# Kernel tuning notes

Measured on AMD Instinct MI355X. Metric: run time of the kernel, lower is better.

## Reference

```python
import jax, jax.numpy as jnp
import numpy as np
from jax import lax

LRELU = 0.1
SQRT_HALF = 0.7071067811865476
DIM = 128
NUM_PRE = 5          # dilated convs in UpsampleNet
NUM_BLOCKS = 3       # WaveNet blocks
LAYERS_PER_BLOCK = 10
NUM_WN = NUM_BLOCKS * LAYERS_PER_BLOCK  # 30


def conv1d(x, w, b, dilation=1):
    # x: [N,C,L], w: [O,I,K], 'same' padding for odd K
    k = w.shape[-1]
    pad = dilation * (k // 2)
    y = lax.conv_general_dilated(
        x, w, window_strides=(1,), padding=[(pad, pad)],
        rhs_dilation=(dilation,), dimension_numbers=('NCW', 'OIW', 'NCW'))
    return y + b[None, :, None]


def conv_transpose1d(x, w, b, stride=4):
    # kernel 4, stride 4, no padding -> L_out = 4*L
    y = lax.conv_transpose(
        x, w, strides=(stride,), padding='VALID',
        dimension_numbers=('NCW', 'OIW', 'NCW'))
    return y + b[None, :, None]


def setup_inputs() -> dict:
    key = jax.random.key(0)
    ks = iter(jax.random.split(key, 32))
    s = 0.02
    d = {}
    d['mel'] = jax.random.normal(next(ks), (4, 80, 64), jnp.float32)
    d['in_w'] = s * jax.random.normal(next(ks), (DIM, 80, 1), jnp.float32)
    d['in_b'] = jnp.zeros((DIM,), jnp.float32)
    d['pre_ws'] = s * jax.random.normal(next(ks), (NUM_PRE, DIM, DIM, 3), jnp.float32)
    d['pre_bs'] = jnp.zeros((NUM_PRE, DIM), jnp.float32)
    d['up1_w'] = s * jax.random.normal(next(ks), (DIM, DIM, 4), jnp.float32)
    d['up1_b'] = jnp.zeros((DIM,), jnp.float32)
    d['up2_w'] = s * jax.random.normal(next(ks), (DIM, DIM, 4), jnp.float32)
    d['up2_b'] = jnp.zeros((DIM,), jnp.float32)
    d['wn_ws'] = s * jax.random.normal(next(ks), (NUM_WN, 2 * DIM, DIM, 3), jnp.float32)
    d['wn_bs'] = jnp.zeros((NUM_WN, 2 * DIM), jnp.float32)
    d['sk_ws'] = s * jax.random.normal(next(ks), (NUM_WN, DIM, DIM, 1), jnp.float32)
    d['sk_bs'] = jnp.zeros((NUM_WN, DIM), jnp.float32)
    d['out1_w'] = s * jax.random.normal(next(ks), (DIM, DIM, 1), jnp.float32)
    d['out1_b'] = jnp.zeros((DIM,), jnp.float32)
    d['out2_w'] = s * jax.random.normal(next(ks), (DIM, DIM, 1), jnp.float32)
    d['out2_b'] = jnp.zeros((DIM,), jnp.float32)
    d['out3_w'] = s * jax.random.normal(next(ks), (1, DIM, 1), jnp.float32)
    d['out3_b'] = jnp.zeros((1,), jnp.float32)
    return d


def reference(mel, in_w, in_b, pre_ws, pre_bs, up1_w, up1_b, up2_w, up2_b,
              wn_ws, wn_bs, sk_ws, sk_bs,
              out1_w, out1_b, out2_w, out2_b, out3_w, out3_b):
    # ---- UpsampleNet ----
    x = conv1d(mel, in_w, in_b)                       # [N,128,T]
    for i in range(NUM_PRE):
        residual = x
        x = conv1d(x, pre_ws[i], pre_bs[i], dilation=2 ** i)
        x = jax.nn.leaky_relu(x, LRELU)
        x = (x + residual) * SQRT_HALF
    x = jax.nn.leaky_relu(conv_transpose1d(x, up1_w, up1_b), LRELU)
    x = jax.nn.leaky_relu(conv_transpose1d(x, up2_w, up2_b), LRELU)
    N, D, L = x.shape
    x = jnp.broadcast_to(x[:, :, :, None], (N, D, L, 16)).reshape(N, D, L * 16)

    # ---- WaveNet blocks (3 blocks x 10 layers) ----
    skips = jnp.zeros_like(x)
    for li in range(NUM_WN):
        dilation = 2 ** (li % LAYERS_PER_BLOCK)
        residual = x
        g = conv1d(x, wn_ws[li], wn_bs[li], dilation=dilation)  # [N,256,L]
        g_tanh, g_sig = jnp.split(g, 2, axis=1)
        gated = jnp.tanh(g_tanh) * jax.nn.sigmoid(g_sig)
        s = conv1d(gated, sk_ws[li], sk_bs[li])
        skips = skips + s
        x = s + residual

    # ---- Output stack ----
    y = jax.nn.relu(skips)
    y = jax.nn.relu(conv1d(y, out1_w, out1_b))
    y = jax.nn.relu(conv1d(y, out2_w, out2_b))
    y = conv1d(y, out3_w, out3_b)
    return jnp.tanh(y)  # [N,1,L*256]
```

## Files before the change

### kernel.cpp

```cpp
#include <hip/hip_runtime.h>
#include <math.h>

#define LRELU 0.1f
#define SQRT_HALF 0.7071067811865476f

constexpr int T_LEN = 16384;

typedef __attribute__((ext_vector_type(8))) short short8;
typedef __attribute__((ext_vector_type(4))) float f32x4;

union U4S8 { uint4 v; short8 s8; unsigned short us[8]; };

__device__ inline void bsplit(float v, unsigned short& hi, unsigned short& lo) {
    unsigned u = __float_as_uint(v);
    unsigned rh = (u + 0x7FFFu + ((u >> 16) & 1u)) >> 16;
    float fh = __uint_as_float(rh << 16);
    float r = v - fh;
    unsigned u2 = __float_as_uint(r);
    unsigned rl = (u2 + 0x7FFFu + ((u2 >> 16) & 1u)) >> 16;
    hi = (unsigned short)rh; lo = (unsigned short)rl;
}
__device__ inline float b2f(unsigned short s) { return __uint_as_float(((unsigned)s) << 16); }

__device__ inline size_t fidx(int n, int tb, int c, int l) {
    return ((size_t)((n << 10) + tb) * 4 + c) * 64 + l;
}

__device__ inline float fast_gate(float g1, float g2) {
    float ax = fabsf(g1);
    float e = __expf(ax + ax);
    float th = 1.f - 2.f * __builtin_amdgcn_rcpf(e + 1.f);
    th = __uint_as_float(__float_as_uint(th) | (__float_as_uint(g1) & 0x80000000u));
    float sg = __builtin_amdgcn_rcpf(1.f + __expf(-g2));
    return th * sg;
}

__global__ void prep_w3(const float* __restrict__ wn_ws, const float* __restrict__ sk_ws,
                        const float* __restrict__ o1w, const float* __restrict__ o2w,
                        unsigned short* __restrict__ Apk, unsigned short* __restrict__ Spk,
                        unsigned short* __restrict__ Opk1, unsigned short* __restrict__ Opk2)
{
    int b = blockIdx.x, tid = threadIdx.x;
    if (b < 360) {
        __shared__ float sl[256][32];
        int li = b / 12, ks = b % 12;
        int tap = ks >> 2, i0 = (ks & 3) * 32;
        for (int j = tid; j < 8192; j += 256) {
            int o = j >> 5, ii = j & 31;
            sl[o][ii] = wn_ws[((size_t)(li * 256 + o) * 128 + i0 + ii) * 3 + tap];
        }
        __syncthreads();
        size_t obase = ((size_t)(li * 12 + ks)) * 16384;
        for (int e = tid; e < 8192; e += 256) {
            int j = e & 7, l = (e >> 3) & 63, m16 = e >> 9;
            int o = m16 * 16 + (l & 15);
            int ii = 4 * (l >> 4) + (j & 3) + 16 * (j >> 2);
            unsigned short hi, lo; bsplit(sl[o][ii], hi, lo);
            Apk[obase + (size_t)m16 * 1024 + l * 8 + j] = hi;
            Apk[obase + (size_t)m16 * 1024 + 512 + l * 8 + j] = lo;
        }
    } else {
        __shared__ float s2[128][32];
        int bb = b - 360;
        const float* src; unsigned short* dst; int ks2;
        if (bb < 120) { int li = bb / 4; ks2 = bb % 4; src = sk_ws + (size_t)li * 16384; dst = Spk + ((size_t)(li * 4 + ks2)) * 8192; }
        else if (bb < 124) { ks2 = bb - 120; src = o1w; dst = Opk1 + (size_t)ks2 * 8192; }
        else { ks2 = bb - 124; src = o2w; dst = Opk2 + (size_t)ks2 * 8192; }
        int i0 = ks2 * 32;
        for (int j = tid; j < 4096; j += 256) {
            int o = j >> 5, ii = j & 31;
            s2[o][ii] = src[(size_t)o * 128 + i0 + ii];
        }
        __syncthreads();
        for (int e = tid; e < 4096; e += 256) {
            int j = e & 7, l = (e >> 3) & 63, m8 = e >> 9;
            int o = m8 * 16 + (l & 15);
            int ii = 4 * (l >> 4) + (j & 3) + 16 * (j >> 2);
            unsigned short hi, lo; bsplit(s2[o][ii], hi, lo);
            dst[(size_t)m8 * 1024 + l * 8 + j] = hi;
            dst[(size_t)m8 * 1024 + 512 + l * 8 + j] = lo;
        }
    }
}

__global__ void fe_in(const float* __restrict__ mel, const float* __restrict__ w,
                      const float* __restrict__ b, float* __restrict__ out)
{
    __shared__ float mc[80];
    int t = blockIdx.x, n = blockIdx.y, o = threadIdx.x;
    if (o < 80) mc[o] = mel[(n * 80 + o) * 64 + t];
    __syncthreads();
    float acc = b[o];
    #pragma unroll 8
    for (int i = 0; i < 80; i++) acc = fmaf(w[o * 80 + i], mc[i], acc);
    out[((size_t)n * 128 + o) * 64 + t] = acc;
}

__global__ void fe_pre(const float* __restrict__ in, float* __restrict__ out,
                       const float* __restrict__ w, const float* __restrict__ b, int d)
{
    __shared__ float col[3][128];
    int t = blockIdx.x, n = blockIdx.y, o = threadIdx.x;
    #pragma unroll
    for (int s = 0; s < 3; s++) {
        int tt = t + (s - 1) * d;
        col[s][o] = ((unsigned)tt < 64u) ? in[(n * 128 + o) * 64 + tt] : 0.f;
    }
    __syncthreads();
    float acc = b[o];
    const float* wo = w + o * 384;
    #pragma unroll 4
    for (int i = 0; i < 128; i++) {
        acc = fmaf(wo[i * 3 + 0], col[0][i], acc);
        acc = fmaf(wo[i * 3 + 1], col[1][i], acc);
        acc = fmaf(wo[i * 3 + 2], col[2][i], acc);
    }
    float y = acc > 0.f ? acc : LRELU * acc;
    out[(n * 128 + o) * 64 + t] = (y + in[(n * 128 + o) * 64 + t]) * SQRT_HALF;
}

__global__ __launch_bounds__(256, 4)
void fe_up3(const float* __restrict__ in, float* __restrict__ out,
            const float* __restrict__ w, const float* __restrict__ bias, int Lin)
{
    __shared__ float xs[128][16];
    const int n = blockIdx.y, qb = blockIdx.x * 16;
    const int tid = threadIdx.x;
    for (int j = tid; j < 2048; j += 256) {
        int i = j >> 4, qq = j & 15;
        xs[i][qq] = in[(size_t)(n * 128 + i) * Lin + qb + qq];
    }
    __syncthreads();
    const int o = tid & 127, qh = tid >> 7;
    float acc[8][4];
    #pragma unroll
    for (int q = 0; q < 8; q++)
        #pragma unroll
        for (int r = 0; r < 4; r++) acc[q][r] = 0.f;
    const float4* wo = (const float4*)(w + (size_t)o * 512);
    for (int i = 0; i < 128; i++) {
        float4 w4 = wo[i];
        #pragma unroll
        for (int q = 0; q < 8; q++) {
            float xv = xs[i][qh * 8 + q];
            acc[q][0] = fmaf(w4.w, xv, acc[q][0]);
            acc[q][1] = fmaf(w4.z, xv, acc[q][1]);
            acc[q][2] = fmaf(w4.y, xv, acc[q][2]);
            acc[q][3] = fmaf(w4.x, xv, acc[q][3]);
        }
    }
    float bo = bias[o];
    const int Lout = 4 * Lin;
    #pragma unroll
    for (int q = 0; q < 8; q++) {
        float4 v;
        float a0 = acc[q][0] + bo, a1 = acc[q][1] + bo, a2 = acc[q][2] + bo, a3 = acc[q][3] + bo;
        v.x = a0 > 0.f ? a0 : LRELU * a0;
        v.y = a1 > 0.f ? a1 : LRELU * a1;
        v.z = a2 > 0.f ? a2 : LRELU * a2;
        v.w = a3 > 0.f ? a3 : LRELU * a3;
        *(float4*)(out + (size_t)(n * 128 + o) * Lout + (size_t)(qb + qh * 8 + q) * 4) = v;
    }
}

__global__ void fe_repeat_f(const float* __restrict__ x1024,
                            uint4* __restrict__ Xh, uint4* __restrict__ Xl)
{
    __shared__ float sx[128][65];
    const int n = blockIdx.y, tbq = blockIdx.x;
    const int tid = threadIdx.x;
    for (int j = tid; j < 8192; j += 256) {
        int ch = j >> 6, col = j & 63;
        sx[ch][col] = x1024[(size_t)(n * 128 + ch) * 1024 + tbq * 64 + col];
    }
    __syncthreads();
    for (int m = tid; m < 16384; m += 256) {
        int l = m & 63, c = (m >> 6) & 3, tbr = m >> 8;
        U4S8 ho, lo_;
        #pragma unroll
        for (int j = 0; j < 8; j++) {
            int ch = 32 * c + 4 * (l >> 4) + (j & 3) + 16 * (j >> 2);
            unsigned short hi, lo; bsplit(sx[ch][tbr], hi, lo);
            ho.us[j] = hi; lo_.us[j] = lo;
        }
        size_t gi = fidx(n, tbq * 64 + tbr, c, l);
        Xh[gi] = ho.v; Xl[gi] = lo_.v;
    }
}

__global__ __launch_bounds__(256, 4)
void wn_layer(const uint4* __restrict__ Xh, const uint4* __restrict__ Xl,
              uint4* __restrict__ Yh, uint4* __restrict__ Yl,
              const unsigned short* __restrict__ Apk, const float* __restrict__ gb,
              const unsigned short* __restrict__ Spk, const float* __restrict__ skb, int dil)
{
    __shared__ __align__(16) uint4 S[2048];

    const int bxs = ((blockIdx.x & 7) << 5) | (blockIdx.x >> 3);
    const int n = blockIdx.y, tb0 = bxs * 4, t0 = tb0 * 16;
    const int tid = threadIdx.x, lane = tid & 63, wid = tid >> 6;

    f32x4 acc[4][4];
    const f32x4 z4 = {0.f, 0.f, 0.f, 0.f};
    #pragma unroll
    for (int mf = 0; mf < 4; mf++)
        #pragma unroll
        for (int nf = 0; nf < 4; nf++) acc[mf][nf] = z4;

    const short8* ap = (const short8*)Apk;
    const int m16c[4] = {2 * wid, 2 * wid + 1, 8 + 2 * wid, 9 + 2 * wid};

    for (int s = 0; s < 3; s++) {
        const int sh = (s - 1) * dil;
        __syncthreads();
        for (int j = tid; j < 1024; j += 256) {
            int l = j & 63, c = (j >> 6) & 3, nf = j >> 8;
            int t = t0 + nf * 16 + (l & 15) + sh;
            uint4 vh = make_uint4(0u, 0u, 0u, 0u), vl = vh;
            if ((unsigned)t < (unsigned)T_LEN) {
                size_t gi = fidx(n, t >> 4, c, (l & 48) | (t & 15));
                vh = Xh[gi]; vl = Xl[gi];
            }
            S[j] = vh; S[1024 + j] = vl;
        }
        __syncthreads();
        for (int c = 0; c < 4; c++) {
            const int ks = s * 4 + c;
            short8 Ah[4], Al[4];
            #pragma unroll
            for (int mf = 0; mf < 4; mf++) {
                int ib = (ks * 16 + m16c[mf]) * 128 + lane;
                Ah[mf] = ap[ib];
                Al[mf] = ap[ib + 64];
            }
            #pragma unroll
            for (int nf = 0; nf < 4; nf++) {
                U4S8 bh, bl;
                bh.v = S[(nf * 4 + c) * 64 + lane];
                bl.v = S[1024 + (nf * 4 + c) * 64 + lane];
                #pragma unroll
                for (int mf = 0; mf < 4; mf++) {
                    acc[mf][nf] = __builtin_amdgcn_mfma_f32_16x16x32_bf16(Ah[mf], bh.s8, acc[mf][nf], 0, 0, 0);
                    acc[mf][nf] = __builtin_amdgcn_mfma_f32_16x16x32_bf16(Al[mf], bh.s8, acc[mf][nf], 0, 0, 0);
                    acc[mf][nf] = __builtin_amdgcn_mfma_f32_16x16x32_bf16(Ah[mf], bl.s8, acc[mf][nf], 0, 0, 0);
                }
            }
        }
    }
    __syncthreads();

    const int cb = 4 * (lane >> 4);
    float bt[2][4], bsg[2][4];
    #pragma unroll
    for (int mf2 = 0; mf2 < 2; mf2++)
        #pragma unroll
        for (int r = 0; r < 4; r++) {
            int ch = (2 * wid + mf2) * 16 + cb + r;
            bt[mf2][r] = gb[ch];
            bsg[mf2][r] = gb[128 + ch];
        }
    #pragma unroll
    for (int nf = 0; nf < 4; nf++) {
        U4S8 h4, l4;
        #pragma unroll
        for (int mf2 = 0; mf2 < 2; mf2++)
            #pragma unroll
            for (int r = 0; r < 4; r++) {
                float g1 = acc[mf2][nf][r] + bt[mf2][r];
                float g2 = acc[mf2 + 2][nf][r] + bsg[mf2][r];
                float gv = fast_gate(g1, g2);
                unsigned short hi, lo; bsplit(gv, hi, lo);
                h4.us[mf2 * 4 + r] = hi;
                l4.us[mf2 * 4 + r] = lo;
            }
        S[(nf * 4 + wid) * 64 + lane] = h4.v;
        S[1024 + (nf * 4 + wid) * 64 + lane] = l4.v;
    }
    __syncthreads();

    f32x4 acc2[2][4];
    #pragma unroll
    for (int mf2 = 0; mf2 < 2; mf2++)
        #pragma unroll
        for (int nf = 0; nf < 4; nf++) acc2[mf2][nf] = z4;
    const short8* sp = (const short8*)Spk;
    #pragma unroll
    for (int c = 0; c < 4; c++) {
        short8 A2h[2], A2l[2];
        #pragma unroll
        for (int mf2 = 0; mf2 < 2; mf2++) {
            int ib = (c * 8 + 2 * wid + mf2) * 128 + lane;
            A2h[mf2] = sp[ib];
            A2l[mf2] = sp[ib + 64];
        }
        #pragma unroll
        for (int nf = 0; nf < 4; nf++) {
            U4S8 bh, bl;
            bh.v = S[(nf * 4 + c) * 64 + lane];
            bl.v = S[1024 + (nf * 4 + c) * 64 + lane];
            #pragma unroll
            for (int mf2 = 0; mf2 < 2; mf2++) {
                acc2[mf2][nf] = __builtin_amdgcn_mfma_f32_16x16x32_bf16(A2h[mf2], bh.s8, acc2[mf2][nf], 0, 0, 0);
                acc2[mf2][nf] = __builtin_amdgcn_mfma_f32_16x16x32_bf16(A2l[mf2], bh.s8, acc2[mf2][nf], 0, 0, 0);
                acc2[mf2][nf] = __builtin_amdgcn_mfma_f32_16x16x32_bf16(A2h[mf2], bl.s8, acc2[mf2][nf], 0, 0, 0);
            }
        }
    }

    float bo2[2][4];
    #pragma unroll
    for (int mf2 = 0; mf2 < 2; mf2++)
        #pragma unroll
        for (int r = 0; r < 4; r++) bo2[mf2][r] = skb[(2 * wid + mf2) * 16 + cb + r];
    #pragma unroll
    for (int nf = 0; nf < 4; nf++) {
        size_t gi = fidx(n, tb0 + nf, wid, lane);
        U4S8 xh, xl, oh, ol;
        xh.v = Xh[gi]; xl.v = Xl[gi];
        #pragma unroll
        for (int j = 0; j < 8; j++) {
            int mf2 = j >> 2, r = j & 3;
            float xin = b2f(xh.us[j]) + b2f(xl.us[j]);
            float sv = acc2[mf2][nf][r] + bo2[mf2][r];
            unsigned short hi, lo; bsplit(sv + xin, hi, lo);
            oh.us[j] = hi; ol.us[j] = lo;
        }
        Yh[gi] = oh.v; Yl[gi] = ol.v;
    }
}

__global__ __launch_bounds__(256, 2)
void os_fused(const uint4* __restrict__ Fh, const uint4* __restrict__ Fl,
              const uint4* __restrict__ Ih, const uint4* __restrict__ Il,
              const unsigned short* __restrict__ Opk1, const float* __restrict__ o1b,
              const unsigned short* __restrict__ Opk2, const float* __restrict__ o2b,
              const float* __restrict__ o3w, const float* __restrict__ o3b,
              float* __restrict__ out)
{
    __shared__ __align__(16) uint4 SA[2048];
    __shared__ __align__(16) uint4 SB[2048];
    const int n = blockIdx.y, tb0 = blockIdx.x * 4, t0 = tb0 * 16;
    const int tid = threadIdx.x, lane = tid & 63, wid = tid >> 6;
    const int tl = lane & 15, cb = 4 * (lane >> 4);
    const f32x4 z4 = {0.f, 0.f, 0.f, 0.f};
    char* ldsA = (char*)SA;

    for (int j = tid; j < 1024; j += 256) {
        int l = j & 63, c = (j >> 6) & 3, nf = j >> 8;
        size_t gi = fidx(n, tb0 + nf, c, l);
        U4S8 fh, fl, ih, il, ho, lo_;
        fh.v = Fh[gi]; fl.v = Fl[gi]; ih.v = Ih[gi]; il.v = Il[gi];
        #pragma unroll
        for (int e = 0; e < 8; e++) {
            float d = (b2f(fh.us[e]) + b2f(fl.us[e])) - (b2f(ih.us[e]) + b2f(il.us[e]));
            d = fmaxf(d, 0.f);
            unsigned short hi, lo; bsplit(d, hi, lo);
            ho.us[e] = hi; lo_.us[e] = lo;
        }
        SA[j] = ho.v; SA[1024 + j] = lo_.v;
    }
    __syncthreads();

    {
        f32x4 acc[2][4];
        #pragma unroll
        for (int mf2 = 0; mf2 < 2; mf2++)
            #pragma unroll
            for (int nf = 0; nf < 4; nf++) acc[mf2][nf] = z4;
        const short8* op = (const short8*)Opk1;
        #pragma unroll
        for (int c = 0; c < 4; c++) {
            short8 Ah[2], Al[2];
            #pragma unroll
            for (int mf2 = 0; mf2 < 2; mf2++) {
                int ib = (c * 8 + 2 * wid + mf2) * 128 + lane;
                Ah[mf2] = op[ib]; Al[mf2] = op[ib + 64];
            }
            #pragma unroll
            for (int nf = 0; nf < 4; nf++) {
                U4S8 bh, bl;
                bh.v = SA[(nf * 4 + c) * 64 + lane];
                bl.v = SA[1024 + (nf * 4 + c) * 64 + lane];
                #pragma unroll
                for (int mf2 = 0; mf2 < 2; mf2++) {
                    acc[mf2][nf] = __builtin_amdgcn_mfma_f32_16x16x32_bf16(Ah[mf2], bh.s8, acc[mf2][nf], 0, 0, 0);
                    acc[mf2][nf] = __builtin_amdgcn_mfma_f32_16x16x32_bf16(Al[mf2], bh.s8, acc[mf2][nf], 0, 0, 0);
                    acc[mf2][nf] = __builtin_amdgcn_mfma_f32_16x16x32_bf16(Ah[mf2], bl.s8, acc[mf2][nf], 0, 0, 0);
                }
            }
        }
        #pragma unroll
        for (int nf = 0; nf < 4; nf++) {
            U4S8 h4, l4;
            #pragma unroll
            for (int mf2 = 0; mf2 < 2; mf2++)
                #pragma unroll
                for (int r = 0; r < 4; r++) {
                    float v = fmaxf(acc[mf2][nf][r] + o1b[(2 * wid + mf2) * 16 + cb + r], 0.f);
                    unsigned short hi, lo; bsplit(v, hi, lo);
                    h4.us[mf2 * 4 + r] = hi; l4.us[mf2 * 4 + r] = lo;
                }
            SB[(nf * 4 + wid) * 64 + lane] = h4.v;
            SB[1024 + (nf * 4 + wid) * 64 + lane] = l4.v;
        }
    }
    __syncthreads();

    {
        f32x4 acc[2][4];
        #pragma unroll
        for (int mf2 = 0; mf2 < 2; mf2++)
            #pragma unroll
            for (int nf = 0; nf < 4; nf++) acc[mf2][nf] = z4;
        const short8* op = (const short8*)Opk2;
        #pragma unroll
        for (int c = 0; c < 4; c++) {
            short8 Ah[2], Al[2];
            #pragma unroll
            for (int mf2 = 0; mf2 < 2; mf2++) {
                int ib = (c * 8 + 2 * wid + mf2) * 128 + lane;
                Ah[mf2] = op[ib]; Al[mf2] = op[ib + 64];
            }
            #pragma unroll
            for (int nf = 0; nf < 4; nf++) {
                U4S8 bh, bl;
                bh.v = SB[(nf * 4 + c) * 64 + lane];
                bl.v = SB[1024 + (nf * 4 + c) * 64 + lane];
                #pragma unroll
                for (int mf2 = 0; mf2 < 2; mf2++) {
                    acc[mf2][nf] = __builtin_amdgcn_mfma_f32_16x16x32_bf16(Ah[mf2], bh.s8, acc[mf2][nf], 0, 0, 0);
                    acc[mf2][nf] = __builtin_amdgcn_mfma_f32_16x16x32_bf16(Al[mf2], bh.s8, acc[mf2][nf], 0, 0, 0);
                    acc[mf2][nf] = __builtin_amdgcn_mfma_f32_16x16x32_bf16(Ah[mf2], bl.s8, acc[mf2][nf], 0, 0, 0);
                }
            }
        }
        __syncthreads();
        #pragma unroll
        for (int mf2 = 0; mf2 < 2; mf2++) {
            const int ch0 = (2 * wid + mf2) * 16 + cb;
            #pragma unroll
            for (int nf = 0; nf < 4; nf++) {
                int row = nf * 16 + tl, swz = (row & 7) << 4;
                float4 v;
                v.x = fmaxf(acc[mf2][nf][0] + o2b[ch0 + 0], 0.f);
                v.y = fmaxf(acc[mf2][nf][1] + o2b[ch0 + 1], 0.f);
                v.z = fmaxf(acc[mf2][nf][2] + o2b[ch0 + 2], 0.f);
                v.w = fmaxf(acc[mf2][nf][3] + o2b[ch0 + 3], 0.f);
                *(float4*)(ldsA + row * 512 + ((ch0 * 4) ^ swz)) = v;
            }
        }
    }
    __syncthreads();

    {
        const int t_loc = tid >> 2, qq = tid & 3;
        const int row = t_loc, swz = (row & 7) << 4;
        float a = 0.f;
        #pragma unroll
        for (int cc = 0; cc < 8; cc++) {
            int ch = qq * 32 + cc * 4;
            float4 v = *(const float4*)(ldsA + row * 512 + ((ch * 4) ^ swz));
            a += o3w[ch] * v.x + o3w[ch + 1] * v.y + o3w[ch + 2] * v.z + o3w[ch + 3] * v.w;
        }
        a += __shfl_xor(a, 1);
        a += __shfl_xor(a, 2);
        if (qq == 0) out[(size_t)n * T_LEN + t0 + t_loc] = tanhf(a + o3b[0]);
    }
}

extern "C" void kernel_launch(void* const* d_in, const int* in_sizes, int n_in,
                              void* d_out, int out_size, void* d_ws, size_t ws_size,
                              hipStream_t stream)
{
    (void)in_sizes; (void)n_in; (void)out_size; (void)ws_size;
    const float* mel    = (const float*)d_in[0];
    const float* in_w   = (const float*)d_in[1];
    const float* in_b   = (const float*)d_in[2];
    const float* pre_w  = (const float*)d_in[3];
    const float* pre_b  = (const float*)d_in[4];
    const float* up1_w  = (const float*)d_in[5];
    const float* up1_b  = (const float*)d_in[6];
    const float* up2_w  = (const float*)d_in[7];
    const float* up2_b  = (const float*)d_in[8];
    const float* wn_wsp = (const float*)d_in[9];
    const float* wn_bs  = (const float*)d_in[10];
    const float* sk_wsp = (const float*)d_in[11];
    const float* sk_bs  = (const float*)d_in[12];
    const float* o1w = (const float*)d_in[13];
    const float* o1b = (const float*)d_in[14];
    const float* o2w = (const float*)d_in[15];
    const float* o2b = (const float*)d_in[16];
    const float* o3w = (const float*)d_in[17];
    const float* o3b = (const float*)d_in[18];

    char* base = (char*)d_ws;
    uint4* XAh = (uint4*)(base);
    uint4* XAl = (uint4*)(base + 16777216);
    uint4* XBh = (uint4*)(base + 33554432);
    uint4* XBl = (uint4*)(base + 50331648);
    uint4* XCh = (uint4*)(base + 67108864);
    uint4* XCl = (uint4*)(base + 83886080);
    unsigned short* Apk = (unsigned short*)(base + 100663296);
    unsigned short* Spk = (unsigned short*)(base + 112459776);
    unsigned short* Opk1 = (unsigned short*)(base + 114425856);
    unsigned short* Opk2 = (unsigned short*)(base + 114491392);
    float* a64   = (float*)(base + 114556928);
    float* b64   = (float*)(base + 114688000);
    float* x256  = (float*)(base + 114819072);
    float* x1024 = (float*)(base + 115343360);

    prep_w3<<<488, 256, 0, stream>>>(wn_wsp, sk_wsp, o1w, o2w, Apk, Spk, Opk1, Opk2);

    fe_in<<<dim3(64, 4), 128, 0, stream>>>(mel, in_w, in_b, a64);
    fe_pre<<<dim3(64, 4), 128, 0, stream>>>(a64, b64, pre_w + 0 * 49152, pre_b + 0 * 128, 1);
    fe_pre<<<dim3(64, 4), 128, 0, stream>>>(b64, a64, pre_w + 1 * 49152, pre_b + 1 * 128, 2);
    fe_pre<<<dim3(64, 4), 128, 0, stream>>>(a64, b64, pre_w + 2 * 49152, pre_b + 2 * 128, 4);
    fe_pre<<<dim3(64, 4), 128, 0, stream>>>(b64, a64, pre_w + 3 * 49152, pre_b + 3 * 128, 8);
    fe_pre<<<dim3(64, 4), 128, 0, stream>>>(a64, b64, pre_w + 4 * 49152, pre_b + 4 * 128, 16);
    fe_up3<<<dim3(4, 4), 256, 0, stream>>>(b64, x256, up1_w, up1_b, 64);
    fe_up3<<<dim3(16, 4), 256, 0, stream>>>(x256, x1024, up2_w, up2_b, 256);
    fe_repeat_f<<<dim3(16, 4), 256, 0, stream>>>(x1024, XAh, XAl);

    for (int li = 0; li < 30; li++) {
        int d = 1 << (li % 10);
        const uint4 *ih, *il; uint4 *oh, *ol;
        if (li == 0)      { ih = XAh; il = XAl; oh = XBh; ol = XBl; }
        else if (li & 1)  { ih = XBh; il = XBl; oh = XCh; ol = XCl; }
        else              { ih = XCh; il = XCl; oh = XBh; ol = XBl; }
        wn_layer<<<dim3(T_LEN / 64, 4), 256, 0, stream>>>(
            ih, il, oh, ol,
            Apk + (size_t)li * 196608, wn_bs + li * 256,
            Spk + (size_t)li * 32768, sk_bs + li * 128, d);
    }

    os_fused<<<dim3(T_LEN / 64, 4), 256, 0, stream>>>(
        XCh, XCl, XAh, XAl, Opk1, o1b, Opk2, o2b, o3w, o3b, (float*)d_out);
}
```

Measured before the change: 1.887 ms.

## Switch WaveNet GEMMs to 32x32x16 MFMA with retiled layout and direct loads for large dilations

Repacks activations and weights into a 32-time by 16-channel fragment layout and replaces the 16x16x32 bf16 MFMA tiles with 32x32x16 tiles in the WaveNet layer and output kernels. The larger tiles cut the fragment loads and instructions issued per unit of work. For dilations of 32 or more, where shifts line up with 32-sample tiles, the layer reads B operands straight from global memory and skips the LDS staging and its barriers. The trade-off is higher accumulator register pressure and uncoalesced global reads on the direct path.

```diff
diff --git a/kernel.cpp b/kernel.cpp
--- a/kernel.cpp
+++ b/kernel.cpp
@@ -7,7 +7,7 @@
 constexpr int T_LEN = 16384;
 
 typedef __attribute__((ext_vector_type(8))) short short8;
-typedef __attribute__((ext_vector_type(4))) float f32x4;
+typedef __attribute__((ext_vector_type(16))) float f32x16;
 
 union U4S8 { uint4 v; short8 s8; unsigned short us[8]; };
 
@@ -22,8 +22,8 @@
 }
 __device__ inline float b2f(unsigned short s) { return __uint_as_float(((unsigned)s) << 16); }
 
-__device__ inline size_t fidx(int n, int tb, int c, int l) {
-    return ((size_t)((n << 10) + tb) * 4 + c) * 64 + l;
+__device__ inline size_t fidx32(int n, int tq, int ic, int l) {
+    return ((size_t)((n << 9) + tq) * 8 + ic) * 64 + l;
 }
 
 __device__ inline float fast_gate(float g1, float g2) {
@@ -41,44 +41,44 @@
                         unsigned short* __restrict__ Opk1, unsigned short* __restrict__ Opk2)
 {
     int b = blockIdx.x, tid = threadIdx.x;
-    if (b < 360) {
-        __shared__ float sl[256][32];
-        int li = b / 12, ks = b % 12;
-        int tap = ks >> 2, i0 = (ks & 3) * 32;
-        for (int j = tid; j < 8192; j += 256) {
-            int o = j >> 5, ii = j & 31;
+    if (b < 720) {
+        __shared__ float sl[256][17];
+        int li = b / 24, ks = b % 24;
+        int tap = ks >> 3, i0 = (ks & 7) * 16;
+        for (int j = tid; j < 4096; j += 256) {
+            int o = j >> 4, ii = j & 15;
             sl[o][ii] = wn_ws[((size_t)(li * 256 + o) * 128 + i0 + ii) * 3 + tap];
         }
         __syncthreads();
-        size_t obase = ((size_t)(li * 12 + ks)) * 16384;
-        for (int e = tid; e < 8192; e += 256) {
-            int j = e & 7, l = (e >> 3) & 63, m16 = e >> 9;
-            int o = m16 * 16 + (l & 15);
-            int ii = 4 * (l >> 4) + (j & 3) + 16 * (j >> 2);
+        size_t obase = ((size_t)(li * 24 + ks)) * 8192;
+        for (int e = tid; e < 4096; e += 256) {
+            int j = e & 7, l = (e >> 3) & 63, ct = e >> 9;
+            int o = ct * 32 + (l & 31);
+            int ii = 4 * (l >> 5) + (j & 3) + 8 * (j >> 2);
             unsigned short hi, lo; bsplit(sl[o][ii], hi, lo);
-            Apk[obase + (size_t)m16 * 1024 + l * 8 + j] = hi;
-            Apk[obase + (size_t)m16 * 1024 + 512 + l * 8 + j] = lo;
+            Apk[obase + (size_t)ct * 1024 + l * 8 + j] = hi;
+            Apk[obase + (size_t)ct * 1024 + 512 + l * 8 + j] = lo;
         }
     } else {
-        __shared__ float s2[128][32];
-        int bb = b - 360;
+        __shared__ float s2[128][17];
+        int bb = b - 720;
         const float* src; unsigned short* dst; int ks2;
-        if (bb < 120) { int li = bb / 4; ks2 = bb % 4; src = sk_ws + (size_t)li * 16384; dst = Spk + ((size_t)(li * 4 + ks2)) * 8192; }
-        else if (bb < 124) { ks2 = bb - 120; src = o1w; dst = Opk1 + (size_t)ks2 * 8192; }
-        else { ks2 = bb - 124; src = o2w; dst = Opk2 + (size_t)ks2 * 8192; }
-        int i0 = ks2 * 32;
-        for (int j = tid; j < 4096; j += 256) {
-            int o = j >> 5, ii = j & 31;
+        if (bb < 240) { int li = bb / 8; ks2 = bb % 8; src = sk_ws + (size_t)li * 16384; dst = Spk + ((size_t)(li * 8 + ks2)) * 4096; }
+        else if (bb < 248) { ks2 = bb - 240; src = o1w; dst = Opk1 + (size_t)ks2 * 4096; }
+        else { ks2 = bb - 248; src = o2w; dst = Opk2 + (size_t)ks2 * 4096; }
+        int i0 = ks2 * 16;
+        for (int j = tid; j < 2048; j += 256) {
+            int o = j >> 4, ii = j & 15;
             s2[o][ii] = src[(size_t)o * 128 + i0 + ii];
         }
         __syncthreads();
-        for (int e = tid; e < 4096; e += 256) {
-            int j = e & 7, l = (e >> 3) & 63, m8 = e >> 9;
-            int o = m8 * 16 + (l & 15);
-            int ii = 4 * (l >> 4) + (j & 3) + 16 * (j >> 2);
+        for (int e = tid; e < 2048; e += 256) {
+            int j = e & 7, l = (e >> 3) & 63, ct = e >> 9;
+            int o = ct * 32 + (l & 31);
+            int ii = 4 * (l >> 5) + (j & 3) + 8 * (j >> 2);
             unsigned short hi, lo; bsplit(s2[o][ii], hi, lo);
-            dst[(size_t)m8 * 1024 + l * 8 + j] = hi;
-            dst[(size_t)m8 * 1024 + 512 + l * 8 + j] = lo;
+            dst[(size_t)ct * 1024 + l * 8 + j] = hi;
+            dst[(size_t)ct * 1024 + 512 + l * 8 + j] = lo;
         }
     }
 }
@@ -175,15 +175,16 @@
     }
     __syncthreads();
     for (int m = tid; m < 16384; m += 256) {
-        int l = m & 63, c = (m >> 6) & 3, tbr = m >> 8;
+        int l = m & 63, ic = (m >> 6) & 7, tqr = m >> 9;
+        int tl = tqr * 32 + (l & 31);
         U4S8 ho, lo_;
         #pragma unroll
         for (int j = 0; j < 8; j++) {
-            int ch = 32 * c + 4 * (l >> 4) + (j & 3) + 16 * (j >> 2);
-            unsigned short hi, lo; bsplit(sx[ch][tbr], hi, lo);
+            int ch = 16 * ic + 4 * (l >> 5) + (j & 3) + 8 * (j >> 2);
+            unsigned short hi, lo; bsplit(sx[ch][tl >> 4], hi, lo);
             ho.us[j] = hi; lo_.us[j] = lo;
         }
-        size_t gi = fidx(n, tbq * 64 + tbr, c, l);
+        size_t gi = fidx32(n, tbq * 32 + tqr, ic, l);
         Xh[gi] = ho.v; Xl[gi] = lo_.v;
     }
 }
@@ -197,135 +198,145 @@
     __shared__ __align__(16) uint4 S[2048];
 
     const int bxs = ((blockIdx.x & 7) << 5) | (blockIdx.x >> 3);
-    const int n = blockIdx.y, tb0 = bxs * 4, t0 = tb0 * 16;
-    const int tid = threadIdx.x, lane = tid & 63, wid = tid >> 6;
-
-    f32x4 acc[4][4];
-    const f32x4 z4 = {0.f, 0.f, 0.f, 0.f};
-    #pragma unroll
-    for (int mf = 0; mf < 4; mf++)
-        #pragma unroll
-        for (int nf = 0; nf < 4; nf++) acc[mf][nf] = z4;
+    const int n = blockIdx.y, tq0 = bxs * 2, t0 = tq0 * 32;
+    const int tid = threadIdx.x, lane = tid & 63, w = tid >> 6;
+    const bool direct = (dil >= 32);
+    const int dq = dil >> 5;
+
+    f32x16 acc[2][2];
+    #pragma unroll
+    for (int ci = 0; ci < 2; ci++)
+        #pragma unroll
+        for (int tt = 0; tt < 2; tt++)
+            #pragma unroll
+            for (int r = 0; r < 16; r++) acc[ci][tt][r] = 0.f;
 
     const short8* ap = (const short8*)Apk;
-    const int m16c[4] = {2 * wid, 2 * wid + 1, 8 + 2 * wid, 9 + 2 * wid};
 
     for (int s = 0; s < 3; s++) {
-        const int sh = (s - 1) * dil;
-        __syncthreads();
-        for (int j = tid; j < 1024; j += 256) {
-            int l = j & 63, c = (j >> 6) & 3, nf = j >> 8;
-            int t = t0 + nf * 16 + (l & 15) + sh;
-            uint4 vh = make_uint4(0u, 0u, 0u, 0u), vl = vh;
-            if ((unsigned)t < (unsigned)T_LEN) {
-                size_t gi = fidx(n, t >> 4, c, (l & 48) | (t & 15));
-                vh = Xh[gi]; vl = Xl[gi];
-            }
-            S[j] = vh; S[1024 + j] = vl;
-        }
-        __syncthreads();
-        for (int c = 0; c < 4; c++) {
-            const int ks = s * 4 + c;
-            short8 Ah[4], Al[4];
-            #pragma unroll
-            for (int mf = 0; mf < 4; mf++) {
-                int ib = (ks * 16 + m16c[mf]) * 128 + lane;
-                Ah[mf] = ap[ib];
-                Al[mf] = ap[ib + 64];
-            }
-            #pragma unroll
-            for (int nf = 0; nf < 4; nf++) {
+        if (!direct) {
+            const int sh = (s - 1) * dil;
+            __syncthreads();
+            for (int j = tid; j < 2048; j += 256) {
+                int p = j >> 10, r = j & 1023, l = r & 63, ic = (r >> 6) & 7, tt = r >> 9;
+                int t = t0 + tt * 32 + (l & 31) + sh;
+                uint4 v = make_uint4(0u, 0u, 0u, 0u);
+                if ((unsigned)t < (unsigned)T_LEN)
+                    v = (p ? Xl : Xh)[fidx32(n, t >> 5, ic, (l & 32) | (t & 31))];
+                S[j] = v;
+            }
+            __syncthreads();
+        }
+        for (int k8 = 0; k8 < 8; k8++) {
+            const int ks = s * 8 + k8;
+            short8 Ah[2], Al[2];
+            #pragma unroll
+            for (int ci = 0; ci < 2; ci++) {
+                int ib = ((ks * 8 + (w + 4 * ci)) * 2) * 64 + lane;
+                Ah[ci] = ap[ib];
+                Al[ci] = ap[ib + 64];
+            }
+            #pragma unroll
+            for (int tt = 0; tt < 2; tt++) {
                 U4S8 bh, bl;
-                bh.v = S[(nf * 4 + c) * 64 + lane];
-                bl.v = S[1024 + (nf * 4 + c) * 64 + lane];
-                #pragma unroll
-                for (int mf = 0; mf < 4; mf++) {
-                    acc[mf][nf] = __builtin_amdgcn_mfma_f32_16x16x32_bf16(Ah[mf], bh.s8, acc[mf][nf], 0, 0, 0);
-                    acc[mf][nf] = __builtin_amdgcn_mfma_f32_16x16x32_bf16(Al[mf], bh.s8, acc[mf][nf], 0, 0, 0);
-                    acc[mf][nf] = __builtin_amdgcn_mfma_f32_16x16x32_bf16(Ah[mf], bl.s8, acc[mf][nf], 0, 0, 0);
+                bool ok = true;
+                if (direct) {
+                    int tq = tq0 + tt + (s - 1) * dq;
+                    ok = ((unsigned)tq < 512u);
+                    if (ok) {
+                        size_t gi = fidx32(n, tq, k8, lane);
+                        bh.v = Xh[gi]; bl.v = Xl[gi];
+                    }
+                } else {
+                    bh.v = S[(tt * 8 + k8) * 64 + lane];
+                    bl.v = S[1024 + (tt * 8 + k8) * 64 + lane];
                 }
-            }
-        }
-    }
-    __syncthreads();
-
-    const int cb = 4 * (lane >> 4);
-    float bt[2][4], bsg[2][4];
-    #pragma unroll
-    for (int mf2 = 0; mf2 < 2; mf2++)
-        #pragma unroll
-        for (int r = 0; r < 4; r++) {
-            int ch = (2 * wid + mf2) * 16 + cb + r;
-            bt[mf2][r] = gb[ch];
-            bsg[mf2][r] = gb[128 + ch];
-        }
-    #pragma unroll
-    for (int nf = 0; nf < 4; nf++) {
-        U4S8 h4, l4;
-        #pragma unroll
-        for (int mf2 = 0; mf2 < 2; mf2++)
-            #pragma unroll
-            for (int r = 0; r < 4; r++) {
-                float g1 = acc[mf2][nf][r] + bt[mf2][r];
-                float g2 = acc[mf2 + 2][nf][r] + bsg[mf2][r];
-                float gv = fast_gate(g1, g2);
+                if (ok) {
+                    #pragma unroll
+                    for (int ci = 0; ci < 2; ci++) {
+                        acc[ci][tt] = __builtin_amdgcn_mfma_f32_32x32x16_bf16(Ah[ci], bh.s8, acc[ci][tt], 0, 0, 0);
+                        acc[ci][tt] = __builtin_amdgcn_mfma_f32_32x32x16_bf16(Al[ci], bh.s8, acc[ci][tt], 0, 0, 0);
+                        acc[ci][tt] = __builtin_amdgcn_mfma_f32_32x32x16_bf16(Ah[ci], bl.s8, acc[ci][tt], 0, 0, 0);
+                    }
+                }
+            }
+        }
+    }
+    if (!direct) __syncthreads();
+
+    const int rsel = 4 * (lane >> 5);
+    float4 btv[4], bsv[4];
+    #pragma unroll
+    for (int rg = 0; rg < 4; rg++) {
+        btv[rg] = *(const float4*)(gb + 32 * w + rg * 8 + rsel);
+        bsv[rg] = *(const float4*)(gb + 128 + 32 * w + rg * 8 + rsel);
+    }
+    #pragma unroll
+    for (int tt = 0; tt < 2; tt++) {
+        #pragma unroll
+        for (int g2 = 0; g2 < 2; g2++) {
+            U4S8 h4, l4;
+            #pragma unroll
+            for (int jj = 0; jj < 8; jj++) {
+                int reg = g2 * 8 + jj;
+                int rg = reg >> 2, e = reg & 3;
+                float bt = (e == 0) ? btv[rg].x : (e == 1) ? btv[rg].y : (e == 2) ? btv[rg].z : btv[rg].w;
+                float bs = (e == 0) ? bsv[rg].x : (e == 1) ? bsv[rg].y : (e == 2) ? bsv[rg].z : bsv[rg].w;
+                float gv = fast_gate(acc[0][tt][reg] + bt, acc[1][tt][reg] + bs);
                 unsigned short hi, lo; bsplit(gv, hi, lo);
-                h4.us[mf2 * 4 + r] = hi;
-                l4.us[mf2 * 4 + r] = lo;
-            }
-        S[(nf * 4 + wid) * 64 + lane] = h4.v;
-        S[1024 + (nf * 4 + wid) * 64 + lane] = l4.v;
-    }
-    __syncthreads();
-
-    f32x4 acc2[2][4];
-    #pragma unroll
-    for (int mf2 = 0; mf2 < 2; mf2++)
-        #pragma unroll
-        for (int nf = 0; nf < 4; nf++) acc2[mf2][nf] = z4;
+                h4.us[jj] = hi; l4.us[jj] = lo;
+            }
+            S[(tt * 8 + 2 * w + g2) * 64 + lane] = h4.v;
+            S[1024 + (tt * 8 + 2 * w + g2) * 64 + lane] = l4.v;
+        }
+    }
+    __syncthreads();
+
+    f32x16 acc2[2];
+    #pragma unroll
+    for (int tt = 0; tt < 2; tt++)
+        #pragma unroll
+        for (int r = 0; r < 16; r++) acc2[tt][r] = 0.f;
     const short8* sp = (const short8*)Spk;
     #pragma unroll
-    for (int c = 0; c < 4; c++) {
-        short8 A2h[2], A2l[2];
-        #pragma unroll
-        for (int mf2 = 0; mf2 < 2; mf2++) {
-            int ib = (c * 8 + 2 * wid + mf2) * 128 + lane;
-            A2h[mf2] = sp[ib];
-            A2l[mf2] = sp[ib + 64];
-        }
-        #pragma unroll
-        for (int nf = 0; nf < 4; nf++) {
+    for (int ks = 0; ks < 8; ks++) {
+        int ib = ((ks * 4 + w) * 2) * 64 + lane;
+        short8 A2h = sp[ib];
+        short8 A2l = sp[ib + 64];
+        #pragma unroll
+        for (int tt = 0; tt < 2; tt++) {
             U4S8 bh, bl;
-            bh.v = S[(nf * 4 + c) * 64 + lane];
-            bl.v = S[1024 + (nf * 4 + c) * 64 + lane];
-            #pragma unroll
-            for (int mf2 = 0; mf2 < 2; mf2++) {
-                acc2[mf2][nf] = __builtin_amdgcn_mfma_f32_16x16x32_bf16(A2h[mf2], bh.s8, acc2[mf2][nf], 0, 0, 0);
-                acc2[mf2][nf] = __builtin_amdgcn_mfma_f32_16x16x32_bf16(A2l[mf2], bh.s8, acc2[mf2][nf], 0, 0, 0);
-                acc2[mf2][nf] = __builtin_amdgcn_mfma_f32_16x16x32_bf16(A2h[mf2], bl.s8, acc2[mf2][nf], 0, 0, 0);
-            }
-        }
-    }
-
-    float bo2[2][4];
-    #pragma unroll
-    for (int mf2 = 0; mf2 < 2; mf2++)
-        #pragma unroll
-        for (int r = 0; r < 4; r++) bo2[mf2][r] = skb[(2 * wid + mf2) * 16 + cb + r];
-    #pragma unroll
-    for (int nf = 0; nf < 4; nf++) {
-        size_t gi = fidx(n, tb0 + nf, wid, lane);
-        U4S8 xh, xl, oh, ol;
-        xh.v = Xh[gi]; xl.v = Xl[gi];
-        #pragma unroll
-        for (int j = 0; j < 8; j++) {
-            int mf2 = j >> 2, r = j & 3;
-            float xin = b2f(xh.us[j]) + b2f(xl.us[j]);
-            float sv = acc2[mf2][nf][r] + bo2[mf2][r];
-            unsigned short hi, lo; bsplit(sv + xin, hi, lo);
-            oh.us[j] = hi; ol.us[j] = lo;
-        }
-        Yh[gi] = oh.v; Yl[gi] = ol.v;
+            bh.v = S[(tt * 8 + ks) * 64 + lane];
+            bl.v = S[1024 + (tt * 8 + ks) * 64 + lane];
+            acc2[tt] = __builtin_amdgcn_mfma_f32_32x32x16_bf16(A2h, bh.s8, acc2[tt], 0, 0, 0);
+            acc2[tt] = __builtin_amdgcn_mfma_f32_32x32x16_bf16(A2l, bh.s8, acc2[tt], 0, 0, 0);
+            acc2[tt] = __builtin_amdgcn_mfma_f32_32x32x16_bf16(A2h, bl.s8, acc2[tt], 0, 0, 0);
+        }
+    }
+
+    float4 skv[4];
+    #pragma unroll
+    for (int rg = 0; rg < 4; rg++)
+        skv[rg] = *(const float4*)(skb + 32 * w + rg * 8 + rsel);
+    #pragma unroll
+    for (int tt = 0; tt < 2; tt++) {
+        #pragma unroll
+        for (int g2 = 0; g2 < 2; g2++) {
+            size_t gi = fidx32(n, tq0 + tt, 2 * w + g2, lane);
+            U4S8 xh, xl, oh, ol;
+            xh.v = Xh[gi]; xl.v = Xl[gi];
+            #pragma unroll
+            for (int jj = 0; jj < 8; jj++) {
+                int reg = g2 * 8 + jj;
+                int rg = reg >> 2, e = reg & 3;
+                float bo = (e == 0) ? skv[rg].x : (e == 1) ? skv[rg].y : (e == 2) ? skv[rg].z : skv[rg].w;
+                float xin = b2f(xh.us[jj]) + b2f(xl.us[jj]);
+                float sv = acc2[tt][reg] + bo;
+                unsigned short hi, lo; bsplit(sv + xin, hi, lo);
+                oh.us[jj] = hi; ol.us[jj] = lo;
+            }
+            Yh[gi] = oh.v; Yl[gi] = ol.v;
+        }
     }
 }
 
@@ -339,15 +350,14 @@
 {
     __shared__ __align__(16) uint4 SA[2048];
     __shared__ __align__(16) uint4 SB[2048];
-    const int n = blockIdx.y, tb0 = blockIdx.x * 4, t0 = tb0 * 16;
-    const int tid = threadIdx.x, lane = tid & 63, wid = tid >> 6;
-    const int tl = lane & 15, cb = 4 * (lane >> 4);
-    const f32x4 z4 = {0.f, 0.f, 0.f, 0.f};
+    const int n = blockIdx.y, tq0 = blockIdx.x * 2, t0 = tq0 * 32;
+    const int tid = threadIdx.x, lane = tid & 63, w = tid >> 6;
+    const int rsel = 4 * (lane >> 5);
     char* ldsA = (char*)SA;
 
     for (int j = tid; j < 1024; j += 256) {
-        int l = j & 63, c = (j >> 6) & 3, nf = j >> 8;
-        size_t gi = fidx(n, tb0 + nf, c, l);
+        int l = j & 63, ic = (j >> 6) & 7, tt = j >> 9;
+        size_t gi = fidx32(n, tq0 + tt, ic, l);
         U4S8 fh, fl, ih, il, ho, lo_;
         fh.v = Fh[gi]; fl.v = Fl[gi]; ih.v = Ih[gi]; il.v = Il[gi];
         #pragma unroll
@@ -362,91 +372,89 @@
     __syncthreads();
 
     {
-        f32x4 acc[2][4];
-        #pragma unroll
-        for (int mf2 = 0; mf2 < 2; mf2++)
-            #pragma unroll
-            for (int nf = 0; nf < 4; nf++) acc[mf2][nf] = z4;
+        f32x16 acc[2];
+        #pragma unroll
+        for (int tt = 0; tt < 2; tt++)
+            #pragma unroll
+            for (int r = 0; r < 16; r++) acc[tt][r] = 0.f;
         const short8* op = (const short8*)Opk1;
         #pragma unroll
-        for (int c = 0; c < 4; c++) {
-            short8 Ah[2], Al[2];
-            #pragma unroll
-            for (int mf2 = 0; mf2 < 2; mf2++) {
-                int ib = (c * 8 + 2 * wid + mf2) * 128 + lane;
-                Ah[mf2] = op[ib]; Al[mf2] = op[ib + 64];
-            }
-            #pragma unroll
-            for (int nf = 0; nf < 4; nf++) {
+        for (int ks = 0; ks < 8; ks++) {
+            int ib = ((ks * 4 + w) * 2) * 64 + lane;
+            short8 Ah = op[ib], Al = op[ib + 64];
+            #pragma unroll
+            for (int tt = 0; tt < 2; tt++) {
                 U4S8 bh, bl;
-                bh.v = SA[(nf * 4 + c) * 64 + lane];
-                bl.v = SA[1024 + (nf * 4 + c) * 64 + lane];
+                bh.v = SA[(tt * 8 + ks) * 64 + lane];
+                bl.v = SA[1024 + (tt * 8 + ks) * 64 + lane];
+                acc[tt] = __builtin_amdgcn_mfma_f32_32x32x16_bf16(Ah, bh.s8, acc[tt], 0, 0, 0);
+                acc[tt] = __builtin_amdgcn_mfma_f32_32x32x16_bf16(Al, bh.s8, acc[tt], 0, 0, 0);
+                acc[tt] = __builtin_amdgcn_mfma_f32_32x32x16_bf16(Ah, bl.s8, acc[tt], 0, 0, 0);
+            }
+        }
+        float4 b1v[4];
+        #pragma unroll
+        for (int rg = 0; rg < 4; rg++)
+            b1v[rg] = *(const float4*)(o1b + 32 * w + rg * 8 + rsel);
+        #pragma unroll
+        for (int tt = 0; tt < 2; tt++)
+            #pragma unroll
+            for (int g2 = 0; g2 < 2; g2++) {
+                U4S8 h4, l4;
                 #pragma unroll
-                for (int mf2 = 0; mf2 < 2; mf2++) {
-                    acc[mf2][nf] = __builtin_amdgcn_mfma_f32_16x16x32_bf16(Ah[mf2], bh.s8, acc[mf2][nf], 0, 0, 0);
-                    acc[mf2][nf] = __builtin_amdgcn_mfma_f32_16x16x32_bf16(Al[mf2], bh.s8, acc[mf2][nf], 0, 0, 0);
-                    acc[mf2][nf] = __builtin_amdgcn_mfma_f32_16x16x32_bf16(Ah[mf2], bl.s8, acc[mf2][nf], 0, 0, 0);
+                for (int jj = 0; jj < 8; jj++) {
+                    int reg = g2 * 8 + jj;
+                    int rg = reg >> 2, e = reg & 3;
+                    float bo = (e == 0) ? b1v[rg].x : (e == 1) ? b1v[rg].y : (e == 2) ? b1v[rg].z : b1v[rg].w;
+                    float v = fmaxf(acc[tt][reg] + bo, 0.f);
+                    unsigned short hi, lo; bsplit(v, hi, lo);
+                    h4.us[jj] = hi; l4.us[jj] = lo;
                 }
-            }
-        }
-        #pragma unroll
-        for (int nf = 0; nf < 4; nf++) {
-            U4S8 h4, l4;
-            #pragma unroll
-            for (int mf2 = 0; mf2 < 2; mf2++)
-                #pragma unroll
-                for (int r = 0; r < 4; r++) {
-                    float v = fmaxf(acc[mf2][nf][r] + o1b[(2 * wid + mf2) * 16 + cb + r], 0.f);
-                    unsigned short hi, lo; bsplit(v, hi, lo);
-                    h4.us[mf2 * 4 + r] = hi; l4.us[mf2 * 4 + r] = lo;
-                }
-            SB[(nf * 4 + wid) * 64 + lane] = h4.v;
-            SB[1024 + (nf * 4 + wid) * 64 + lane] = l4.v;
-        }
+                SB[(tt * 8 + 2 * w + g2) * 64 + lane] = h4.v;
+                SB[1024 + (tt * 8 + 2 * w + g2) * 64 + lane] = l4.v;
+            }
     }
     __syncthreads();
 
     {
-        f32x4 acc[2][4];
-        #pragma unroll
-        for (int mf2 = 0; mf2 < 2; mf2++)
-            #pragma unroll
-            for (int nf = 0; nf < 4; nf++) acc[mf2][nf] = z4;
+        f32x16 acc[2];
+        #pragma unroll
+        for (int tt = 0; tt < 2; tt++)
+            #pragma unroll
+            for (int r = 0; r < 16; r++) acc[tt][r] = 0.f;
         const short8* op = (const short8*)Opk2;
         #pragma unroll
-        for (int c = 0; c < 4; c++) {
-            short8 Ah[2], Al[2];
-            #pragma unroll
-            for (int mf2 = 0; mf2 < 2; mf2++) {
-                int ib = (c * 8 + 2 * wid + mf2) * 128 + lane;
-                Ah[mf2] = op[ib]; Al[mf2] = op[ib + 64];
-            }
-            #pragma unroll
-            for (int nf = 0; nf < 4; nf++) {
+        for (int ks = 0; ks < 8; ks++) {
+            int ib = ((ks * 4 + w) * 2) * 64 + lane;
+            short8 Ah = op[ib], Al = op[ib + 64];
+            #pragma unroll
+            for (int tt = 0; tt < 2; tt++) {
                 U4S8 bh, bl;
-                bh.v = SB[(nf * 4 + c) * 64 + lane];
-                bl.v = SB[1024 + (nf * 4 + c) * 64 + lane];
-                #pragma unroll
-                for (int mf2 = 0; mf2 < 2; mf2++) {
-                    acc[mf2][nf] = __builtin_amdgcn_mfma_f32_16x16x32_bf16(Ah[mf2], bh.s8, acc[mf2][nf], 0, 0, 0);
-                    acc[mf2][nf] = __builtin_amdgcn_mfma_f32_16x16x32_bf16(Al[mf2], bh.s8, acc[mf2][nf], 0, 0, 0);
-                    acc[mf2][nf] = __builtin_amdgcn_mfma_f32_16x16x32_bf16(Ah[mf2], bl.s8, acc[mf2][nf], 0, 0, 0);
-                }
-            }
-        }
+                bh.v = SB[(tt * 8 + ks) * 64 + lane];
+                bl.v = SB[1024 + (tt * 8 + ks) * 64 + lane];
+                acc[tt] = __builtin_amdgcn_mfma_f32_32x32x16_bf16(Ah, bh.s8, acc[tt], 0, 0, 0);
+                acc[tt] = __builtin_amdgcn_mfma_f32_32x32x16_bf16(Al, bh.s8, acc[tt], 0, 0, 0);
+                acc[tt] = __builtin_amdgcn_mfma_f32_32x32x16_bf16(Ah, bl.s8, acc[tt], 0, 0, 0);
+            }
+        }
+        float4 b2v[4];
+        #pragma unroll
+        for (int rg = 0; rg < 4; rg++)
+            b2v[rg] = *(const float4*)(o2b + 32 * w + rg * 8 + rsel);
         __syncthreads();
         #pragma unroll
-        for (int mf2 = 0; mf2 < 2; mf2++) {
-            const int ch0 = (2 * wid + mf2) * 16 + cb;
-            #pragma unroll
-            for (int nf = 0; nf < 4; nf++) {
-                int row = nf * 16 + tl, swz = (row & 7) << 4;
+        for (int tt = 0; tt < 2; tt++) {
+            int tl = tt * 32 + (lane & 31);
+            int swz = (tl & 7) << 4;
+            #pragma unroll
+            for (int rg = 0; rg < 4; rg++) {
+                int ch0 = 32 * w + rg * 8 + rsel;
                 float4 v;
-                v.x = fmaxf(acc[mf2][nf][0] + o2b[ch0 + 0], 0.f);
-                v.y = fmaxf(acc[mf2][nf][1] + o2b[ch0 + 1], 0.f);
-                v.z = fmaxf(acc[mf2][nf][2] + o2b[ch0 + 2], 0.f);
-                v.w = fmaxf(acc[mf2][nf][3] + o2b[ch0 + 3], 0.f);
-                *(float4*)(ldsA + row * 512 + ((ch0 * 4) ^ swz)) = v;
+                v.x = fmaxf(acc[tt][rg * 4 + 0] + b2v[rg].x, 0.f);
+                v.y = fmaxf(acc[tt][rg * 4 + 1] + b2v[rg].y, 0.f);
+                v.z = fmaxf(acc[tt][rg * 4 + 2] + b2v[rg].z, 0.f);
+                v.w = fmaxf(acc[tt][rg * 4 + 3] + b2v[rg].w, 0.f);
+                *(float4*)(ldsA + tl * 512 + ((ch0 * 4) ^ swz)) = v;
             }
         }
     }
@@ -509,7 +517,7 @@
     float* x256  = (float*)(base + 114819072);
     float* x1024 = (float*)(base + 115343360);
 
-    prep_w3<<<488, 256, 0, stream>>>(wn_wsp, sk_wsp, o1w, o2w, Apk, Spk, Opk1, Opk2);
+    prep_w3<<<976, 256, 0, stream>>>(wn_wsp, sk_wsp, o1w, o2w, Apk, Spk, Opk1, Opk2);
 
     fe_in<<<dim3(64, 4), 128, 0, stream>>>(mel, in_w, in_b, a64);
     fe_pre<<<dim3(64, 4), 128, 0, stream>>>(a64, b64, pre_w + 0 * 49152, pre_b + 0 * 128, 1);
```

After: 1.708 ms. -9.5%, faster.
